# Performance work log

Hardware: AMD Instinct MI355X
Metric: run time of the kernel (lower is better)

Reference implementation:

```python
import jax, jax.numpy as jnp
import numpy as np

N = 50000        # nodes
E = 800000       # random edges (self loops appended inside reference, per PyG default)
IN = 128         # in_channels
H1, C1 = 8, 64   # conv1: heads, hidden_channels
NUM_CLASSES = 2  # conv2 out (heads=1, concat=False)
NEG_SLOPE = 0.2  # PyG GATConv default LeakyReLU slope


def setup_inputs() -> dict:
    key = jax.random.key(0)
    ks = jax.random.split(key, 12)
    x = jax.random.normal(ks[0], (N, IN), dtype=jnp.float32)
    edge_index = jax.random.randint(ks[1], (2, E), 0, N)
    # conv1 params: W1 [IN, H1*C1], att vectors [H1, C1], bias [H1*C1]
    W1 = jax.random.normal(ks[2], (IN, H1 * C1), dtype=jnp.float32) / np.sqrt(IN)
    a_src1 = jax.random.normal(ks[3], (H1, C1), dtype=jnp.float32) / np.sqrt(C1)
    a_dst1 = jax.random.normal(ks[4], (H1, C1), dtype=jnp.float32) / np.sqrt(C1)
    b1 = jnp.zeros((H1 * C1,), dtype=jnp.float32)
    # conv2 params: heads=1, out=NUM_CLASSES
    W2 = jax.random.normal(ks[5], (H1 * C1, 1 * NUM_CLASSES), dtype=jnp.float32) / np.sqrt(H1 * C1)
    a_src2 = jax.random.normal(ks[6], (1, NUM_CLASSES), dtype=jnp.float32) / np.sqrt(NUM_CLASSES)
    a_dst2 = jax.random.normal(ks[7], (1, NUM_CLASSES), dtype=jnp.float32) / np.sqrt(NUM_CLASSES)
    b2 = jnp.zeros((NUM_CLASSES,), dtype=jnp.float32)
    return {"x": x, "edge_index": edge_index, "W1": W1, "a_src1": a_src1,
            "a_dst1": a_dst1, "b1": b1, "W2": W2, "a_src2": a_src2,
            "a_dst2": a_dst2, "b2": b2}


def gat_layer(x, src, dst, W, a_src, a_dst, bias, concat):
    n = x.shape[0]
    heads, ch = a_src.shape
    h = (x @ W).reshape(n, heads, ch)                      # [N,H,C]
    alpha_s = jnp.einsum('nhc,hc->nh', h, a_src)           # per-node src score
    alpha_d = jnp.einsum('nhc,hc->nh', h, a_dst)           # per-node dst score
    e = jax.nn.leaky_relu(alpha_s[src] + alpha_d[dst], NEG_SLOPE)  # [Etot,H]
    # segment softmax over edges grouped by destination node
    m = jax.ops.segment_max(e, dst, num_segments=n)
    ex = jnp.exp(e - m[dst])
    den = jax.ops.segment_sum(ex, dst, num_segments=n)
    alpha = ex / den[dst]                                  # [Etot,H]
    out = jax.ops.segment_sum(h[src] * alpha[:, :, None], dst, num_segments=n)  # [N,H,C]
    out = out.reshape(n, heads * ch) if concat else out.mean(axis=1)
    return out + bias


def reference(x, edge_index, W1, a_src1, a_dst1, b1, W2, a_src2, a_dst2, b2):
    n = x.shape[0]
    loops = jnp.arange(n, dtype=edge_index.dtype)
    src = jnp.concatenate([edge_index[0], loops])   # PyG add_self_loops=True
    dst = jnp.concatenate([edge_index[1], loops])
    h = gat_layer(x, src, dst, W1, a_src1, a_dst1, b1, concat=True)   # [N, H1*C1]
    h = jax.nn.elu(h)
    # dropout is identity in eval mode
    out = gat_layer(h, src, dst, W2, a_src2, a_dst2, b2, concat=False)  # [N, 2]
    return out
```

## Files before the change

### kernel.cpp

```cpp
#include <hip/hip_runtime.h>
#include <hip/hip_bf16.h>

#define NEG 0.2f
#define BKT 64
#define DSTR 32

typedef __attribute__((ext_vector_type(8))) short bf16x8;
typedef __attribute__((ext_vector_type(4))) float f32x4;

static __device__ __forceinline__ unsigned short f2bf(float f) {
    union { float f; unsigned u; } v; v.f = f;
    unsigned r = v.u + 0x7fff + ((v.u >> 16) & 1);
    return (unsigned short)(r >> 16);
}
static __device__ __forceinline__ float bf_lo(unsigned u) {
    return __uint_as_float(u << 16);
}
static __device__ __forceinline__ float bf_hi(unsigned u) {
    return __uint_as_float(u & 0xffff0000u);
}

__global__ void k_init(int* __restrict__ deg, unsigned short* __restrict__ csr,
                       const float* __restrict__ W1, unsigned short* __restrict__ W1bT,
                       int n) {
    int v = blockIdx.x * 256 + threadIdx.x;
    if (v < n) {
        deg[(size_t)v * DSTR] = 1;
        csr[(size_t)v * BKT] = (unsigned short)v;
    }
    int col = v >> 7, row = v & 127;
    W1bT[(size_t)col * 128 + row] = f2bf(W1[(size_t)row * 512 + col]);
}

__global__ __launch_bounds__(256) void k_big(const int* __restrict__ ei,
                                             int* __restrict__ deg,
                                             unsigned short* __restrict__ csr,
                                             const float* __restrict__ x,
                                             const unsigned short* __restrict__ W1bT,
                                             const float* __restrict__ a_src,
                                             const float* __restrict__ a_dst,
                                             unsigned short* __restrict__ h1b,
                                             float* __restrict__ as1,
                                             float* __restrict__ ad1,
                                             int E_, int n, int gblocks) {
    int tid = threadIdx.x;
    if ((int)blockIdx.x >= gblocks) {
        int base = (blockIdx.x - gblocks) * 512 + tid;
        if (base < E_) {
            int s = ei[base], d = ei[E_ + base];
            int slot = atomicAdd(&deg[(size_t)d * DSTR], 1);
            if (slot < BKT) csr[(size_t)d * BKT + slot] = (unsigned short)s;
        }
        int e2 = base + 256;
        if (e2 < E_) {
            int s = ei[e2], d = ei[E_ + e2];
            int slot = atomicAdd(&deg[(size_t)d * DSTR], 1);
            if (slot < BKT) csr[(size_t)d * BKT + slot] = (unsigned short)s;
        }
        return;
    }
    __shared__ unsigned short stg[4][16][72];
    int wave = tid >> 6, lane = tid & 63;
    int l15 = lane & 15, q = lane >> 4;
    int rowblk = blockIdx.x * 128 + wave * 32;

    bf16x8 xf[2][4];
    #pragma unroll
    for (int st = 0; st < 2; st++) {
        int ar = rowblk + st * 16 + l15; if (ar > n - 1) ar = n - 1;
        const float* ap = x + (size_t)ar * 128 + q * 8;
        #pragma unroll
        for (int kb = 0; kb < 4; kb++) {
            float4 v0 = *(const float4*)(ap + kb * 32);
            float4 v1 = *(const float4*)(ap + kb * 32 + 4);
            xf[st][kb][0] = (short)f2bf(v0.x); xf[st][kb][1] = (short)f2bf(v0.y);
            xf[st][kb][2] = (short)f2bf(v0.z); xf[st][kb][3] = (short)f2bf(v0.w);
            xf[st][kb][4] = (short)f2bf(v1.x); xf[st][kb][5] = (short)f2bf(v1.y);
            xf[st][kb][6] = (short)f2bf(v1.z); xf[st][kb][7] = (short)f2bf(v1.w);
        }
    }

    for (int j = 0; j < 8; j++) {
        int col0 = j * 64;
        bf16x8 bfr[4][4];
        #pragma unroll
        for (int kb = 0; kb < 4; kb++)
            #pragma unroll
            for (int t = 0; t < 4; t++)
                bfr[kb][t] = *(const bf16x8*)(W1bT + (size_t)(col0 + t * 16 + l15) * 128
                                              + kb * 32 + q * 8);
        float asv[4], adv[4];
        #pragma unroll
        for (int t = 0; t < 4; t++) {
            asv[t] = a_src[j * 64 + t * 16 + l15];
            adv[t] = a_dst[j * 64 + t * 16 + l15];
        }

        #pragma unroll
        for (int st = 0; st < 2; st++) {
            int row0 = rowblk + st * 16;
            f32x4 acc[4] = {};
            #pragma unroll
            for (int kb = 0; kb < 4; kb++)
                #pragma unroll
                for (int t = 0; t < 4; t++)
                    acc[t] = __builtin_amdgcn_mfma_f32_16x16x32_bf16(xf[st][kb], bfr[kb][t], acc[t], 0, 0, 0);
            #pragma unroll
            for (int t = 0; t < 4; t++)
                #pragma unroll
                for (int r = 0; r < 4; r++)
                    stg[wave][q * 4 + r][t * 16 + l15] = f2bf(acc[t][r]);
            #pragma unroll
            for (int p = 0; p < 2; p++) {
                int lr = p * 8 + (lane >> 3);
                int row = row0 + lr;
                int cd = (lane & 7) * 8;
                uint4 vv = *(const uint4*)&stg[wave][lr][cd];
                if (row < n)
                    *(uint4*)(h1b + (size_t)row * 512 + col0 + cd) = vv;
            }
            float ps[4], pd[4];
            #pragma unroll
            for (int r = 0; r < 4; r++) {
                ps[r] = acc[0][r] * asv[0] + acc[1][r] * asv[1]
                      + acc[2][r] * asv[2] + acc[3][r] * asv[3];
                pd[r] = acc[0][r] * adv[0] + acc[1][r] * adv[1]
                      + acc[2][r] * adv[2] + acc[3][r] * adv[3];
                #pragma unroll
                for (int off = 1; off < 16; off <<= 1) {
                    ps[r] += __shfl_xor(ps[r], off, 64);
                    pd[r] += __shfl_xor(pd[r], off, 64);
                }
            }
            if (l15 < 4) {
                int r = l15;
                float vps = ps[0], vpd = pd[0];
                if (r == 1) { vps = ps[1]; vpd = pd[1]; }
                if (r == 2) { vps = ps[2]; vpd = pd[2]; }
                if (r == 3) { vps = ps[3]; vpd = pd[3]; }
                int row = row0 + q * 4 + r;
                if (row < n) { as1[row * 8 + j] = vps; ad1[row * 8 + j] = vpd; }
            }
        }
    }
}

__global__ __launch_bounds__(256) void k_agg1(const unsigned short* __restrict__ h1b,
                                              const float* __restrict__ as1,
                                              const float* __restrict__ ad1,
                                              const float* __restrict__ b1,
                                              const float* __restrict__ W2,
                                              const int* __restrict__ deg,
                                              const unsigned short* __restrict__ csr,
                                              float* __restrict__ h2, int n) {
    int lane = threadIdx.x & 63;
    int v = blockIdx.x * 4 + (threadIdx.x >> 6);
    if (v >= n) return;
    int head = lane >> 3, c = lane * 8;
    int dv = deg[(size_t)v * DSTR]; if (dv > BKT) dv = BKT;
    const unsigned short* cp = csr + (size_t)v * BKT;
    float adh = ad1[v * 8 + head];
    float s = 0.f;
    float acc[8] = {};
    int i = 0;
    for (; i + 4 <= dv; i += 4) {
        ushort4 uu = *(const ushort4*)(cp + i);
        int u0 = uu.x, u1 = uu.y, u2 = uu.z, u3 = uu.w;
        float ea = as1[u0 * 8 + head] + adh;
        float eb = as1[u1 * 8 + head] + adh;
        float ec = as1[u2 * 8 + head] + adh;
        float ed = as1[u3 * 8 + head] + adh;
        uint4 h0 = *(const uint4*)(h1b + (size_t)u0 * 512 + c);
        uint4 h1 = *(const uint4*)(h1b + (size_t)u1 * 512 + c);
        uint4 h2v = *(const uint4*)(h1b + (size_t)u2 * 512 + c);
        uint4 h3 = *(const uint4*)(h1b + (size_t)u3 * 512 + c);
        ea = (ea >= 0.f) ? ea : NEG * ea;
        eb = (eb >= 0.f) ? eb : NEG * eb;
        ec = (ec >= 0.f) ? ec : NEG * ec;
        ed = (ed >= 0.f) ? ed : NEG * ed;
        float w0 = __expf(ea), w1 = __expf(eb), w2 = __expf(ec), w3 = __expf(ed);
        s += (w0 + w1) + (w2 + w3);
        acc[0] = fmaf(w3, bf_lo(h3.x), fmaf(w2, bf_lo(h2v.x), fmaf(w1, bf_lo(h1.x), fmaf(w0, bf_lo(h0.x), acc[0]))));
        acc[1] = fmaf(w3, bf_hi(h3.x), fmaf(w2, bf_hi(h2v.x), fmaf(w1, bf_hi(h1.x), fmaf(w0, bf_hi(h0.x), acc[1]))));
        acc[2] = fmaf(w3, bf_lo(h3.y), fmaf(w2, bf_lo(h2v.y), fmaf(w1, bf_lo(h1.y), fmaf(w0, bf_lo(h0.y), acc[2]))));
        acc[3] = fmaf(w3, bf_hi(h3.y), fmaf(w2, bf_hi(h2v.y), fmaf(w1, bf_hi(h1.y), fmaf(w0, bf_hi(h0.y), acc[3]))));
        acc[4] = fmaf(w3, bf_lo(h3.z), fmaf(w2, bf_lo(h2v.z), fmaf(w1, bf_lo(h1.z), fmaf(w0, bf_lo(h0.z), acc[4]))));
        acc[5] = fmaf(w3, bf_hi(h3.z), fmaf(w2, bf_hi(h2v.z), fmaf(w1, bf_hi(h1.z), fmaf(w0, bf_hi(h0.z), acc[5]))));
        acc[6] = fmaf(w3, bf_lo(h3.w), fmaf(w2, bf_lo(h2v.w), fmaf(w1, bf_lo(h1.w), fmaf(w0, bf_lo(h0.w), acc[6]))));
        acc[7] = fmaf(w3, bf_hi(h3.w), fmaf(w2, bf_hi(h2v.w), fmaf(w1, bf_hi(h1.w), fmaf(w0, bf_hi(h0.w), acc[7]))));
    }
    for (; i < dv; i++) {
        int u = cp[i];
        float e = as1[u * 8 + head] + adh;
        e = (e >= 0.f) ? e : NEG * e;
        float w = __expf(e);
        s += w;
        uint4 hv = *(const uint4*)(h1b + (size_t)u * 512 + c);
        acc[0] = fmaf(w, bf_lo(hv.x), acc[0]);
        acc[1] = fmaf(w, bf_hi(hv.x), acc[1]);
        acc[2] = fmaf(w, bf_lo(hv.y), acc[2]);
        acc[3] = fmaf(w, bf_hi(hv.y), acc[3]);
        acc[4] = fmaf(w, bf_lo(hv.z), acc[4]);
        acc[5] = fmaf(w, bf_hi(hv.z), acc[5]);
        acc[6] = fmaf(w, bf_lo(hv.w), acc[6]);
        acc[7] = fmaf(w, bf_hi(hv.w), acc[7]);
    }
    float inv = 1.0f / s;
    float4 ba = *(const float4*)(b1 + c);
    float4 bb = *(const float4*)(b1 + c + 4);
    float o[8] = {acc[0] * inv + ba.x, acc[1] * inv + ba.y,
                  acc[2] * inv + ba.z, acc[3] * inv + ba.w,
                  acc[4] * inv + bb.x, acc[5] * inv + bb.y,
                  acc[6] * inv + bb.z, acc[7] * inv + bb.w};
    #pragma unroll
    for (int jj = 0; jj < 8; jj++)
        o[jj] = (o[jj] > 0.f) ? o[jj] : (__expf(o[jj]) - 1.0f);
    const float4* wp = (const float4*)(W2 + c * 2);
    float4 w0 = wp[0], w1 = wp[1], w2 = wp[2], w3 = wp[3];
    float p0 = o[0] * w0.x + o[1] * w0.z + o[2] * w1.x + o[3] * w1.z
             + o[4] * w2.x + o[5] * w2.z + o[6] * w3.x + o[7] * w3.z;
    float p1 = o[0] * w0.y + o[1] * w0.w + o[2] * w1.y + o[3] * w1.w
             + o[4] * w2.y + o[5] * w2.w + o[6] * w3.y + o[7] * w3.w;
    #pragma unroll
    for (int off = 1; off < 64; off <<= 1) {
        p0 += __shfl_xor(p0, off, 64);
        p1 += __shfl_xor(p1, off, 64);
    }
    if (lane == 0) {
        h2[2 * v] = p0;
        h2[2 * v + 1] = p1;
    }
}

__global__ __launch_bounds__(256) void k_agg2(const float* __restrict__ h2,
                                              const float* __restrict__ a_src2,
                                              const float* __restrict__ a_dst2,
                                              const float* __restrict__ b2,
                                              const int* __restrict__ deg,
                                              const unsigned short* __restrict__ csr,
                                              float* __restrict__ out, int n) {
    int tid = threadIdx.x;
    int lane = tid & 63, wave = tid >> 6;
    int sub = lane & 7, g = lane >> 3;
    int v = blockIdx.x * 32 + wave * 8 + g;
    if (v >= n) return;
    int dv = deg[(size_t)v * DSTR]; if (dv > BKT) dv = BKT;
    const unsigned short* cp = csr + (size_t)v * BKT;
    float sa0 = a_src2[0], sa1 = a_src2[1];
    float da0 = a_dst2[0], da1 = a_dst2[1];
    float2 hv = *(const float2*)(h2 + 2 * v);
    float adv = hv.x * da0 + hv.y * da1;
    float s = 0.f, a0 = 0.f, a1 = 0.f;
    for (int i = sub; i < dv; i += 8) {
        int u = cp[i];
        float2 hu = *(const float2*)(h2 + 2 * u);
        float e = hu.x * sa0 + hu.y * sa1 + adv;
        e = (e >= 0.f) ? e : NEG * e;
        float w = __expf(e);
        s += w;
        a0 = fmaf(w, hu.x, a0);
        a1 = fmaf(w, hu.y, a1);
    }
    #pragma unroll
    for (int off = 1; off < 8; off <<= 1) {
        s  += __shfl_xor(s, off, 64);
        a0 += __shfl_xor(a0, off, 64);
        a1 += __shfl_xor(a1, off, 64);
    }
    if (sub == 0) {
        float inv = 1.0f / s;
        out[2 * v]     = a0 * inv + b2[0];
        out[2 * v + 1] = a1 * inv + b2[1];
    }
}

extern "C" void kernel_launch(void* const* d_in, const int* in_sizes, int n_in,
                              void* d_out, int out_size, void* d_ws, size_t ws_size,
                              hipStream_t stream) {
    const float* x      = (const float*)d_in[0];
    const int*   ei     = (const int*)d_in[1];
    const float* W1     = (const float*)d_in[2];
    const float* a_src1 = (const float*)d_in[3];
    const float* a_dst1 = (const float*)d_in[4];
    const float* b1     = (const float*)d_in[5];
    const float* W2     = (const float*)d_in[6];
    const float* a_src2 = (const float*)d_in[7];
    const float* a_dst2 = (const float*)d_in[8];
    const float* b2     = (const float*)d_in[9];
    float* out = (float*)d_out;

    int n  = in_sizes[0] / 128;
    int E_ = in_sizes[1] / 2;
    int rblk = (n + 127) / 128;
    int npad = rblk * 128;

    char* w = (char*)d_ws;
    auto alloc = [&](size_t bytes) {
        char* p = w; w += (bytes + 255) & ~(size_t)255; return p;
    };
    int*            deg    = (int*)alloc((size_t)n * DSTR * 4);
    unsigned short* csr    = (unsigned short*)alloc((size_t)n * BKT * 2);
    unsigned short* h1b    = (unsigned short*)alloc((size_t)npad * 512 * 2);
    unsigned short* W1bT   = (unsigned short*)alloc((size_t)512 * 128 * 2);
    float*          as1    = (float*)alloc((size_t)n * 8 * 4);
    float*          ad1    = (float*)alloc((size_t)n * 8 * 4);
    float*          h2     = (float*)alloc((size_t)n * 2 * 4);

    k_init<<<256, 256, 0, stream>>>(deg, csr, W1, W1bT, n);

    int gblocks = rblk;
    int sblocks = (E_ + 511) / 512;
    k_big<<<gblocks + sblocks, 256, 0, stream>>>(ei, deg, csr, x, W1bT,
                                                 a_src1, a_dst1, h1b, as1, ad1,
                                                 E_, n, gblocks);

    int nb = (n + 3) / 4;
    k_agg1<<<nb, 256, 0, stream>>>(h1b, as1, ad1, b1, W2, deg, csr, h2, n);

    int ab = (n + 31) / 32;
    k_agg2<<<ab, 256, 0, stream>>>(h2, a_src2, a_dst2, b2, deg, csr, out, n);
}
```

Measured before the change: 283.9 us.

## Slice h1 by head pairs and pin slices to XCDs for L2-local gathers

The layer-1 features are stored slice-major: four column slices of 128 bf16 values, two heads each. Blocks of the aggregation kernel are mapped by blockIdx modulo 8 so that each XCD handles only one slice, meant to cut the random-gather working set per XCD L2 to a quarter. Each slice produces partial layer-2 projections, and a new small k_red kernel sums them into h2. In exchange the CSR, degree and attention-score reads are repeated per slice, and there is an extra launch and partial-sum buffer.

```diff
diff --git a/kernel.cpp b/kernel.cpp
--- a/kernel.cpp
+++ b/kernel.cpp
@@ -117,7 +117,7 @@
                 int cd = (lane & 7) * 8;
                 uint4 vv = *(const uint4*)&stg[wave][lr][cd];
                 if (row < n)
-                    *(uint4*)(h1b + (size_t)row * 512 + col0 + cd) = vv;
+                    *(uint4*)(h1b + ((size_t)(j >> 1) * n + row) * 128 + (j & 1) * 64 + cd) = vv;
             }
             float ps[4], pd[4];
             #pragma unroll
@@ -152,14 +152,27 @@
                                               const float* __restrict__ W2,
                                               const int* __restrict__ deg,
                                               const unsigned short* __restrict__ csr,
-                                              float* __restrict__ h2, int n) {
-    int lane = threadIdx.x & 63;
-    int v = blockIdx.x * 4 + (threadIdx.x >> 6);
+                                              float* __restrict__ part,
+                                              int n, int tpx) {
+    int b = blockIdx.x;
+    int xcd = b & 7;
+    int slice = xcd & 3;
+    int half = xcd >> 2;
+    int j = (b >> 3) + half * tpx;
+
+    int tid = threadIdx.x;
+    int lane = tid & 63, wave = tid >> 6;
+    int g = lane >> 4, sub = lane & 15;
+    int v = j * 16 + wave * 4 + g;
     if (v >= n) return;
-    int head = lane >> 3, c = lane * 8;
+
+    int head = slice * 2 + (sub >> 3);
+    int c = sub * 8;
+    const unsigned short* hb = h1b + (size_t)slice * n * 128 + c;
     int dv = deg[(size_t)v * DSTR]; if (dv > BKT) dv = BKT;
     const unsigned short* cp = csr + (size_t)v * BKT;
     float adh = ad1[v * 8 + head];
+
     float s = 0.f;
     float acc[8] = {};
     int i = 0;
@@ -170,10 +183,10 @@
         float eb = as1[u1 * 8 + head] + adh;
         float ec = as1[u2 * 8 + head] + adh;
         float ed = as1[u3 * 8 + head] + adh;
-        uint4 h0 = *(const uint4*)(h1b + (size_t)u0 * 512 + c);
-        uint4 h1 = *(const uint4*)(h1b + (size_t)u1 * 512 + c);
-        uint4 h2v = *(const uint4*)(h1b + (size_t)u2 * 512 + c);
-        uint4 h3 = *(const uint4*)(h1b + (size_t)u3 * 512 + c);
+        uint4 h0 = *(const uint4*)(hb + (size_t)u0 * 128);
+        uint4 h1 = *(const uint4*)(hb + (size_t)u1 * 128);
+        uint4 h2v = *(const uint4*)(hb + (size_t)u2 * 128);
+        uint4 h3 = *(const uint4*)(hb + (size_t)u3 * 128);
         ea = (ea >= 0.f) ? ea : NEG * ea;
         eb = (eb >= 0.f) ? eb : NEG * eb;
         ec = (ec >= 0.f) ? ec : NEG * ec;
@@ -195,7 +208,7 @@
         e = (e >= 0.f) ? e : NEG * e;
         float w = __expf(e);
         s += w;
-        uint4 hv = *(const uint4*)(h1b + (size_t)u * 512 + c);
+        uint4 hv = *(const uint4*)(hb + (size_t)u * 128);
         acc[0] = fmaf(w, bf_lo(hv.x), acc[0]);
         acc[1] = fmaf(w, bf_hi(hv.x), acc[1]);
         acc[2] = fmaf(w, bf_lo(hv.y), acc[2]);
@@ -205,31 +218,40 @@
         acc[6] = fmaf(w, bf_lo(hv.w), acc[6]);
         acc[7] = fmaf(w, bf_hi(hv.w), acc[7]);
     }
+
     float inv = 1.0f / s;
-    float4 ba = *(const float4*)(b1 + c);
-    float4 bb = *(const float4*)(b1 + c + 4);
-    float o[8] = {acc[0] * inv + ba.x, acc[1] * inv + ba.y,
-                  acc[2] * inv + ba.z, acc[3] * inv + ba.w,
-                  acc[4] * inv + bb.x, acc[5] * inv + bb.y,
-                  acc[6] * inv + bb.z, acc[7] * inv + bb.w};
-    #pragma unroll
-    for (int jj = 0; jj < 8; jj++)
-        o[jj] = (o[jj] > 0.f) ? o[jj] : (__expf(o[jj]) - 1.0f);
-    const float4* wp = (const float4*)(W2 + c * 2);
-    float4 w0 = wp[0], w1 = wp[1], w2 = wp[2], w3 = wp[3];
-    float p0 = o[0] * w0.x + o[1] * w0.z + o[2] * w1.x + o[3] * w1.z
-             + o[4] * w2.x + o[5] * w2.z + o[6] * w3.x + o[7] * w3.z;
-    float p1 = o[0] * w0.y + o[1] * w0.w + o[2] * w1.y + o[3] * w1.w
-             + o[4] * w2.y + o[5] * w2.w + o[6] * w3.y + o[7] * w3.w;
-    #pragma unroll
-    for (int off = 1; off < 64; off <<= 1) {
+    int cb = slice * 128 + c;
+    float p0 = 0.f, p1 = 0.f;
+    #pragma unroll
+    for (int k2 = 0; k2 < 8; k2++) {
+        float o = acc[k2] * inv + b1[cb + k2];
+        o = (o > 0.f) ? o : (__expf(o) - 1.0f);
+        p0 = fmaf(o, W2[(cb + k2) * 2], p0);
+        p1 = fmaf(o, W2[(cb + k2) * 2 + 1], p1);
+    }
+    #pragma unroll
+    for (int off = 1; off < 16; off <<= 1) {
         p0 += __shfl_xor(p0, off, 64);
         p1 += __shfl_xor(p1, off, 64);
     }
-    if (lane == 0) {
-        h2[2 * v] = p0;
-        h2[2 * v + 1] = p1;
-    }
+    if (sub == 0) {
+        float* pp = part + ((size_t)slice * n + v) * 2;
+        pp[0] = p0;
+        pp[1] = p1;
+    }
+}
+
+__global__ void k_red(const float* __restrict__ part, float* __restrict__ h2, int n) {
+    int v = blockIdx.x * 256 + threadIdx.x;
+    if (v >= n) return;
+    float s0 = 0.f, s1 = 0.f;
+    #pragma unroll
+    for (int p = 0; p < 4; p++) {
+        float2 pv = *(const float2*)(part + ((size_t)p * n + v) * 2);
+        s0 += pv.x; s1 += pv.y;
+    }
+    h2[2 * v] = s0;
+    h2[2 * v + 1] = s1;
 }
 
 __global__ __launch_bounds__(256) void k_agg2(const float* __restrict__ h2,
@@ -292,7 +314,6 @@
     int n  = in_sizes[0] / 128;
     int E_ = in_sizes[1] / 2;
     int rblk = (n + 127) / 128;
-    int npad = rblk * 128;
 
     char* w = (char*)d_ws;
     auto alloc = [&](size_t bytes) {
@@ -300,10 +321,11 @@
     };
     int*            deg    = (int*)alloc((size_t)n * DSTR * 4);
     unsigned short* csr    = (unsigned short*)alloc((size_t)n * BKT * 2);
-    unsigned short* h1b    = (unsigned short*)alloc((size_t)npad * 512 * 2);
+    unsigned short* h1b    = (unsigned short*)alloc((size_t)n * 4 * 128 * 2);
     unsigned short* W1bT   = (unsigned short*)alloc((size_t)512 * 128 * 2);
     float*          as1    = (float*)alloc((size_t)n * 8 * 4);
     float*          ad1    = (float*)alloc((size_t)n * 8 * 4);
+    float*          part   = (float*)alloc((size_t)n * 4 * 2 * 4);
     float*          h2     = (float*)alloc((size_t)n * 2 * 4);
 
     k_init<<<256, 256, 0, stream>>>(deg, csr, W1, W1bT, n);
@@ -314,8 +336,13 @@
                                                  a_src1, a_dst1, h1b, as1, ad1,
                                                  E_, n, gblocks);
 
-    int nb = (n + 3) / 4;
-    k_agg1<<<nb, 256, 0, stream>>>(h1b, as1, ad1, b1, W2, deg, csr, h2, n);
+    int nblk16 = (n + 15) / 16;
+    int tpx = (nblk16 + 1) / 2;
+    k_agg1<<<8 * tpx, 256, 0, stream>>>(h1b, as1, ad1, b1, W2, deg, csr,
+                                        part, n, tpx);
+
+    int nb256 = (n + 255) / 256;
+    k_red<<<nb256, 256, 0, stream>>>(part, h2, n);
 
     int ab = (n + 31) / 32;
     k_agg2<<<ab, 256, 0, stream>>>(h2, a_src2, a_dst2, b2, deg, csr, out, n);
```

Measured after the change: 286.2 us. No clear change (+0.8%).
